# Performance work log

Measured on AMD Instinct MI355X. Metric: run time of the kernel, lower is better.

## Reference

```python
import jax, jax.numpy as jnp
import numpy as np

B, N, D, QM, QP, NP, T = 16, 900, 256, 4, 4, 6, 4


def setup_inputs() -> dict:
    key = jax.random.key(0)
    ks = jax.random.split(key, 12)
    return {
        "motion_query": jax.random.normal(ks[0], (B, N, D), jnp.float32),
        "plan_query": jax.random.normal(ks[1], (B, NP, D), jnp.float32),
        "ego_status_feature": jax.random.normal(ks[2], (B, D), jnp.float32),
        "motion_queue": jax.random.normal(ks[3], (B, QM, N, D), jnp.float32),
        "plan_queue": jax.random.normal(ks[4], (B, QP, NP, D), jnp.float32),
        "ego_status_queue": jax.random.normal(ks[5], (B, QP, D), jnp.float32),
        "period": jax.random.randint(ks[6], (B, QM), 0, 4, jnp.int32),
        "mask": jax.random.bernoulli(ks[7], 0.9, (B,)),
        "temp_anchor_embed_forstate": jax.random.normal(ks[8], (B, N, T, D), jnp.float32),
        "temp_mask_forstate": jax.random.bernoulli(ks[9], 0.5, (B, N, T)),
        "ego_temp_anchor_embed_forstate": jax.random.normal(ks[10], (B, 1, T, D), jnp.float32),
        "ego_temp_mask_forstate": jax.random.bernoulli(ks[11], 0.5, (B, 1, T)),
    }


def reference(motion_query, plan_query, ego_status_feature, motion_queue,
              plan_queue, ego_status_queue, period, mask,
              temp_anchor_embed_forstate, temp_mask_forstate,
              ego_temp_anchor_embed_forstate, ego_temp_mask_forstate):
    sg = jax.lax.stop_gradient
    # --- masked queue reset: for batch rows with mask==False, overwrite every
    # queue entry with the (detached) current value and zero the period ---
    reset = ~mask  # [B]
    mq = jnp.where(reset[:, None, None, None], sg(motion_query)[:, None], motion_queue)
    pq = jnp.where(reset[:, None, None, None], sg(plan_query)[:, None], plan_queue)
    eq = jnp.where(reset[:, None, None], sg(ego_status_feature)[:, None], ego_status_queue)
    per = jnp.where(reset[:, None], 0, period)

    # --- temporal window: T == 4, so both branches take the simple slice ---
    mm = temp_mask_forstate[..., :-1]            # [B, N, T-1]
    me = temp_anchor_embed_forstate[..., :-1, :]  # [B, N, T-1, D]
    pm = ego_temp_mask_forstate[..., :-1]         # [B, 1, T-1]
    pe = ego_temp_anchor_embed_forstate[..., :-1, :]  # [B, 1, T-1, D]

    # --- propagate plan embed forward over masked prefix ---
    any_flag = jnp.any(pm)
    all_true = jnp.all(pm, axis=(-2, -1))                # [B]
    m1 = pm[:, 0, :]                                     # [B, T-1] (Np == 1)
    first_false = jnp.argmin(m1, axis=-1)                # [B] index of first False
    Tm1 = pm.shape[-1]
    # embed at first-False slot (else branch) vs last-frame ego embed (all-True)
    repl_else = jnp.take_along_axis(pe, first_false[:, None, None, None], axis=2)[:, :, 0, :]
    repl_all = ego_temp_anchor_embed_forstate[:, :, -1, :]
    repl = jnp.where(all_true[:, None, None], repl_all, repl_else)  # [B, 1, D]
    j = jnp.arange(Tm1)
    overwrite = all_true[:, None] | (j[None, :] < first_false[:, None])  # [B, T-1]
    pe = jnp.where(any_flag & overwrite[:, None, :, None], repl[:, :, None, :], pe)

    return (mq, pq, eq, per,
            mm.swapaxes(1, 2), me.swapaxes(1, 2),
            pm.swapaxes(1, 2), pe.swapaxes(1, 2))
```

## Files before the change

### kernel.cpp

```cpp
#include <hip/hip_runtime.h>
#include <stdint.h>

namespace {
constexpr int Bn = 16, Nn = 900, Dn = 256, QMn = 4, QPn = 4, NPn = 6, Tn = 4;

constexpr int SZ_MQ  = Bn * QMn * Nn * Dn;
constexpr int SZ_PQ  = Bn * QPn * NPn * Dn;
constexpr int SZ_EQ  = Bn * QPn * Dn;
constexpr int SZ_PER = Bn * QMn;
constexpr int SZ_MM  = Bn * (Tn - 1) * Nn;
constexpr int SZ_ME  = Bn * (Tn - 1) * Nn * Dn;
constexpr int SZ_PM  = Bn * (Tn - 1);
constexpr int SZ_PE  = Bn * (Tn - 1) * Dn;

constexpr int OFF_MQ  = 0;
constexpr int OFF_PQ  = OFF_MQ + SZ_MQ;
constexpr int OFF_EQ  = OFF_PQ + SZ_PQ;
constexpr int OFF_PER = OFF_EQ + SZ_EQ;
constexpr int OFF_MM  = OFF_PER + SZ_PER;
constexpr int OFF_ME  = OFF_MM + SZ_MM;
constexpr int OFF_PM  = OFF_ME + SZ_ME;
constexpr int OFF_PE  = OFF_PM + SZ_PM;
constexpr int TOTAL   = OFF_PE + SZ_PE;
constexpr int NPACKS  = TOTAL / 8;
}

using u16 = unsigned short;

__device__ __forceinline__ float bits_to_f(unsigned u) {
    return __builtin_bit_cast(float, u);
}

__device__ int detect_float_mode(const void* p) {
    const unsigned* w = (const unsigned*)p;
    int cnt = 0;
#pragma unroll
    for (int i = 0; i < 32; ++i) {
        unsigned ex = (w[i] >> 7) & 0xFFu;
        cnt += (ex >= 120u && ex <= 133u) ? 1 : 0;
    }
    return (cnt >= 16) ? 1 : 0;
}

enum { BM_I32 = 0, BM_U8 = 1, BM_BF16 = 2, BM_F32 = 3 };
__device__ int detect_bool_mode(const void* p) {
    const unsigned* w = (const unsigned*)p;
    unsigned orw = 0, or_even = 0;
    bool hw_ok = true, u8_ok = true;
#pragma unroll
    for (int i = 0; i < 64; ++i) {
        unsigned x = w[i];
        orw |= x;
        unsigned lo = x & 0xFFFFu, hi = x >> 16;
        hw_ok = hw_ok && (lo == 0u || lo == 0x3F80u) && (hi == 0u || hi == 0x3F80u);
        or_even |= lo;
        u8_ok = u8_ok && ((x & 0xFEFEFEFEu) == 0u);
    }
    if (orw <= 1u) return BM_I32;
    if (hw_ok)     return (or_even == 0u) ? BM_F32 : BM_BF16;
    if (u8_ok)     return BM_U8;
    return BM_I32;
}

__device__ __forceinline__ bool get_bool(const void* p, int i, int m) {
    if (m == BM_I32) return ((const int*)p)[i] != 0;
    if (m == BM_U8)  return ((const unsigned char*)p)[i] != 0;
    if (m == BM_BF16) return ((const u16*)p)[i] != 0;
    return ((const unsigned*)p)[i] != 0;
}

__device__ int detect_period_mode(const void* p) {
    const unsigned* w = (const unsigned*)p;
    unsigned orw = 0, or_even = 0;
    bool hw_ok = true;
#pragma unroll
    for (int i = 0; i < 16; ++i) {
        unsigned x = w[i];
        orw |= x;
        unsigned lo = x & 0xFFFFu, hi = x >> 16;
        bool lo_ok = (lo == 0u || lo == 0x3F80u || lo == 0x4000u || lo == 0x4040u);
        bool hi_ok = (hi == 0u || hi == 0x3F80u || hi == 0x4000u || hi == 0x4040u);
        hw_ok = hw_ok && lo_ok && hi_ok;
        or_even |= lo;
    }
    if (orw <= 3u) return 0;
    if (hw_ok && or_even == 0u) return 2;
    return 1;
}

__device__ __forceinline__ float get_period_f(const void* p, int i, int m) {
    if (m == 0) return (float)((const int*)p)[i];
    if (m == 1) return bits_to_f((unsigned)((const u16*)p)[i] << 16);
    return ((const float*)p)[i];
}

__device__ __forceinline__ void load8f(const void* base, int e, int fm,
                                       float4& A, float4& B) {
    if (fm == 0) {
        const float* f = (const float*)base + e;
        A = reinterpret_cast<const float4*>(f)[0];
        B = reinterpret_cast<const float4*>(f)[1];
    } else {
        const int4 r = *reinterpret_cast<const int4*>((const u16*)base + e);
        unsigned x;
        x = (unsigned)r.x; A.x = bits_to_f(x << 16); A.y = bits_to_f(x & 0xFFFF0000u);
        x = (unsigned)r.y; A.z = bits_to_f(x << 16); A.w = bits_to_f(x & 0xFFFF0000u);
        x = (unsigned)r.z; B.x = bits_to_f(x << 16); B.y = bits_to_f(x & 0xFFFF0000u);
        x = (unsigned)r.w; B.z = bits_to_f(x << 16); B.w = bits_to_f(x & 0xFFFF0000u);
    }
}

__device__ __forceinline__ void compute_pack(
    int pack, int fm, int bm, int pmode,
    const void* __restrict__ motion_query,
    const void* __restrict__ plan_query,
    const void* __restrict__ ego_status_feature,
    const void* __restrict__ motion_queue,
    const void* __restrict__ plan_queue,
    const void* __restrict__ ego_status_queue,
    const void* __restrict__ period,
    const void* __restrict__ mask,
    const void* __restrict__ temp_anchor,
    const void* __restrict__ temp_mask,
    const void* __restrict__ ego_anchor,
    const void* __restrict__ ego_mask,
    float4& A, float4& B)
{
    const int idx = pack * 8;

    if (idx < OFF_PQ) {
        const int e = idx - OFF_MQ;
        const int d = e & (Dn - 1);
        const unsigned row = (unsigned)(e >> 8);
        const unsigned bq = row / (unsigned)Nn;
        const unsigned n = row - bq * (unsigned)Nn;
        const unsigned b = bq >> 2;
        const bool reset = !get_bool(mask, (int)b, bm);
        if (reset) load8f(motion_query, (((int)b * Nn + (int)n) << 8) + d, fm, A, B);
        else       load8f(motion_queue, e, fm, A, B);
    } else if (idx < OFF_EQ) {
        const int e = idx - OFF_PQ;
        const int d = e & (Dn - 1);
        const unsigned row = (unsigned)(e >> 8);
        const unsigned b = row / (unsigned)(QPn * NPn);
        const unsigned rem = row - b * (unsigned)(QPn * NPn);
        const unsigned q = rem / (unsigned)NPn;
        const unsigned p = rem - q * (unsigned)NPn;
        const bool reset = !get_bool(mask, (int)b, bm);
        if (reset) load8f(plan_query, (((int)b * NPn + (int)p) << 8) + d, fm, A, B);
        else       load8f(plan_queue, e, fm, A, B);
    } else if (idx < OFF_PER) {
        const int e = idx - OFF_EQ;
        const int d = e & (Dn - 1);
        const int row = e >> 8;
        const int b = row >> 2;
        const bool reset = !get_bool(mask, b, bm);
        if (reset) load8f(ego_status_feature, (b << 8) + d, fm, A, B);
        else       load8f(ego_status_queue, e, fm, A, B);
    } else if (idx < OFF_MM) {
        const int e = idx - OFF_PER;
        float h[8];
#pragma unroll
        for (int k = 0; k < 8; ++k) {
            const int g = e + k;
            const int b = g >> 2;
            const bool reset = !get_bool(mask, b, bm);
            h[k] = reset ? 0.0f : get_period_f(period, g, pmode);
        }
        A = make_float4(h[0], h[1], h[2], h[3]);
        B = make_float4(h[4], h[5], h[6], h[7]);
    } else if (idx < OFF_ME) {
        const int e = idx - OFF_MM;
        float h[8];
#pragma unroll
        for (int k = 0; k < 8; ++k) {
            const unsigned g = (unsigned)(e + k);
            const unsigned b = g / (unsigned)((Tn - 1) * Nn);
            const unsigned rem = g - b * (unsigned)((Tn - 1) * Nn);
            const unsigned t = rem / (unsigned)Nn;
            const unsigned n = rem - t * (unsigned)Nn;
            h[k] = get_bool(temp_mask, ((int)b * Nn + (int)n) * Tn + (int)t, bm)
                       ? 1.0f : 0.0f;
        }
        A = make_float4(h[0], h[1], h[2], h[3]);
        B = make_float4(h[4], h[5], h[6], h[7]);
    } else if (idx < OFF_PM) {
        const int e = idx - OFF_ME;
        const int d = e & (Dn - 1);
        const unsigned row = (unsigned)(e >> 8);
        const unsigned b = row / (unsigned)((Tn - 1) * Nn);
        const unsigned rem = row - b * (unsigned)((Tn - 1) * Nn);
        const unsigned t = rem / (unsigned)Nn;
        const unsigned n = rem - t * (unsigned)Nn;
        load8f(temp_anchor, ((((int)b * Nn + (int)n) * Tn + (int)t) << 8) + d, fm, A, B);
    } else if (idx < OFF_PE) {
        const int e = idx - OFF_PM;
        float h[8];
#pragma unroll
        for (int k = 0; k < 8; ++k) {
            const unsigned g = (unsigned)(e + k);
            const unsigned b = g / (unsigned)(Tn - 1);
            const unsigned t = g - b * (unsigned)(Tn - 1);
            h[k] = get_bool(ego_mask, (int)b * Tn + (int)t, bm) ? 1.0f : 0.0f;
        }
        A = make_float4(h[0], h[1], h[2], h[3]);
        B = make_float4(h[4], h[5], h[6], h[7]);
    } else {
        const int e = idx - OFF_PE;
        const int d = e & (Dn - 1);
        const unsigned row = (unsigned)(e >> 8);
        const unsigned b = row / (unsigned)(Tn - 1);
        const unsigned t = row - b * (unsigned)(Tn - 1);

        bool any_flag = false;
#pragma unroll
        for (int bb = 0; bb < Bn; ++bb) {
            any_flag = any_flag || get_bool(ego_mask, bb * Tn + 0, bm)
                                || get_bool(ego_mask, bb * Tn + 1, bm)
                                || get_bool(ego_mask, bb * Tn + 2, bm);
        }

        const bool p0 = get_bool(ego_mask, (int)b * Tn + 0, bm);
        const bool p1 = get_bool(ego_mask, (int)b * Tn + 1, bm);
        const bool p2 = get_bool(ego_mask, (int)b * Tn + 2, bm);
        const bool all_true = p0 && p1 && p2;
        const int first_false = (!p0) ? 0 : ((!p1) ? 1 : ((!p2) ? 2 : 0));

        const bool overwrite = all_true || ((int)t < first_false);
        int src_t = (int)t;
        if (any_flag && overwrite) src_t = all_true ? (Tn - 1) : first_false;

        load8f(ego_anchor, (((int)b * Tn + src_t) << 8) + d, fm, A, B);
    }
}

__global__ __launch_bounds__(256) void state_queue_kernel(
    const void* __restrict__ motion_query,
    const void* __restrict__ plan_query,
    const void* __restrict__ ego_status_feature,
    const void* __restrict__ motion_queue,
    const void* __restrict__ plan_queue,
    const void* __restrict__ ego_status_queue,
    const void* __restrict__ period,
    const void* __restrict__ mask,
    const void* __restrict__ temp_anchor,
    const void* __restrict__ temp_mask,
    const void* __restrict__ ego_anchor,
    const void* __restrict__ ego_mask,
    float* __restrict__ out)
{
    __shared__ int s_modes[3];
    if (threadIdx.x == 0) {
        s_modes[0] = detect_float_mode(motion_query);
        s_modes[1] = detect_bool_mode(temp_mask);
        s_modes[2] = detect_period_mode(period);
    }
    __syncthreads();
    const int fm = s_modes[0];
    const int bm = s_modes[1];
    const int pmode = s_modes[2];

    const int stride = (int)(gridDim.x * blockDim.x);

    for (int pack = (int)(blockIdx.x * blockDim.x + threadIdx.x);
         pack < NPACKS; pack += stride) {
        float4 A, B;
        compute_pack(pack, fm, bm, pmode,
                     motion_query, plan_query, ego_status_feature, motion_queue,
                     plan_queue, ego_status_queue, period, mask, temp_anchor,
                     temp_mask, ego_anchor, ego_mask, A, B);
        reinterpret_cast<float4*>(out + pack * 8)[0] = A;
        reinterpret_cast<float4*>(out + pack * 8)[1] = B;
    }
}

extern "C" void kernel_launch(void* const* d_in, const int* in_sizes, int n_in,
                              void* d_out, int out_size, void* d_ws, size_t ws_size,
                              hipStream_t stream) {
    float* out = (float*)d_out;
    const int threads = 256;
    const int blocks = 4096;
    state_queue_kernel<<<blocks, threads, 0, stream>>>(
        d_in[0], d_in[1], d_in[2], d_in[3], d_in[4], d_in[5], d_in[6], d_in[7],
        d_in[8], d_in[9], d_in[10], d_in[11], out);
}
```

Baseline: 226.0 us.

## Specialize blocks per output region instead of one grid-stride branchy loop

Replaces the uniform grid-stride loop, which ran a long branch chain for every pack, with a grid partitioned by region. One set of blocks copies the motion queue, another copies the temporal anchor embeds, each thread handling three packs at a fixed stride, and 64 blocks cover the small sections. This removes per-pack region dispatch and divergence on the two large copies and sizes the grid to the work. The small sections are handled by only 64 blocks, which may leave them lightly parallelized.

```diff
diff --git a/kernel.cpp b/kernel.cpp
--- a/kernel.cpp
+++ b/kernel.cpp
@@ -22,7 +22,15 @@
 constexpr int OFF_PM  = OFF_ME + SZ_ME;
 constexpr int OFF_PE  = OFF_PM + SZ_PM;
 constexpr int TOTAL   = OFF_PE + SZ_PE;
-constexpr int NPACKS  = TOTAL / 8;
+
+constexpr int MQ_BLOCKS    = SZ_MQ / 6144;
+constexpr int ME_BLOCKS    = SZ_ME / 6144;
+constexpr int SMALL_BLOCKS = 64;
+constexpr int NUM_BLOCKS   = MQ_BLOCKS + ME_BLOCKS + SMALL_BLOCKS;
+
+constexpr int SMALL1       = OFF_ME - OFF_PQ;
+constexpr int SMALL_TOTAL  = SMALL1 + (TOTAL - OFF_PM);
+constexpr int SMALL_PACKS  = SMALL_TOTAL / 8;
 }
 
 using u16 = unsigned short;
@@ -110,35 +118,20 @@
     }
 }
 
-__device__ __forceinline__ void compute_pack(
-    int pack, int fm, int bm, int pmode,
-    const void* __restrict__ motion_query,
+__device__ void compute_pack_small(
+    int idx, int fm, int bm, int pmode,
     const void* __restrict__ plan_query,
     const void* __restrict__ ego_status_feature,
-    const void* __restrict__ motion_queue,
     const void* __restrict__ plan_queue,
     const void* __restrict__ ego_status_queue,
     const void* __restrict__ period,
     const void* __restrict__ mask,
-    const void* __restrict__ temp_anchor,
     const void* __restrict__ temp_mask,
     const void* __restrict__ ego_anchor,
     const void* __restrict__ ego_mask,
     float4& A, float4& B)
 {
-    const int idx = pack * 8;
-
-    if (idx < OFF_PQ) {
-        const int e = idx - OFF_MQ;
-        const int d = e & (Dn - 1);
-        const unsigned row = (unsigned)(e >> 8);
-        const unsigned bq = row / (unsigned)Nn;
-        const unsigned n = row - bq * (unsigned)Nn;
-        const unsigned b = bq >> 2;
-        const bool reset = !get_bool(mask, (int)b, bm);
-        if (reset) load8f(motion_query, (((int)b * Nn + (int)n) << 8) + d, fm, A, B);
-        else       load8f(motion_queue, e, fm, A, B);
-    } else if (idx < OFF_EQ) {
+    if (idx < OFF_EQ) {
         const int e = idx - OFF_PQ;
         const int d = e & (Dn - 1);
         const unsigned row = (unsigned)(e >> 8);
@@ -184,15 +177,6 @@
         }
         A = make_float4(h[0], h[1], h[2], h[3]);
         B = make_float4(h[4], h[5], h[6], h[7]);
-    } else if (idx < OFF_PM) {
-        const int e = idx - OFF_ME;
-        const int d = e & (Dn - 1);
-        const unsigned row = (unsigned)(e >> 8);
-        const unsigned b = row / (unsigned)((Tn - 1) * Nn);
-        const unsigned rem = row - b * (unsigned)((Tn - 1) * Nn);
-        const unsigned t = rem / (unsigned)Nn;
-        const unsigned n = rem - t * (unsigned)Nn;
-        load8f(temp_anchor, ((((int)b * Nn + (int)n) * Tn + (int)t) << 8) + d, fm, A, B);
     } else if (idx < OFF_PE) {
         const int e = idx - OFF_PM;
         float h[8];
@@ -260,17 +244,57 @@
     const int bm = s_modes[1];
     const int pmode = s_modes[2];
 
-    const int stride = (int)(gridDim.x * blockDim.x);
-
-    for (int pack = (int)(blockIdx.x * blockDim.x + threadIdx.x);
-         pack < NPACKS; pack += stride) {
-        float4 A, B;
-        compute_pack(pack, fm, bm, pmode,
-                     motion_query, plan_query, ego_status_feature, motion_queue,
-                     plan_queue, ego_status_queue, period, mask, temp_anchor,
-                     temp_mask, ego_anchor, ego_mask, A, B);
-        reinterpret_cast<float4*>(out + pack * 8)[0] = A;
-        reinterpret_cast<float4*>(out + pack * 8)[1] = B;
+    const int bx  = (int)blockIdx.x;
+    const int tid = (int)threadIdx.x;
+
+    if (bx < MQ_BLOCKS) {
+        const int p0 = bx * 768 + tid;
+#pragma unroll
+        for (int it = 0; it < 3; ++it) {
+            const int e = (p0 + it * 256) * 8;
+            const int d = e & (Dn - 1);
+            const unsigned row = (unsigned)(e >> 8);
+            const unsigned bq  = row / (unsigned)Nn;
+            const unsigned n   = row - bq * (unsigned)Nn;
+            const unsigned b   = bq >> 2;
+            const bool keep = get_bool(mask, (int)b, bm);
+            const void* src = keep ? motion_queue : motion_query;
+            const int   off = keep ? e : ((((int)b * Nn + (int)n) << 8) + d);
+            float4 A, Bv;
+            load8f(src, off, fm, A, Bv);
+            reinterpret_cast<float4*>(out + e)[0] = A;
+            reinterpret_cast<float4*>(out + e)[1] = Bv;
+        }
+    } else if (bx < MQ_BLOCKS + ME_BLOCKS) {
+        const int p0 = (bx - MQ_BLOCKS) * 768 + tid;
+#pragma unroll
+        for (int it = 0; it < 3; ++it) {
+            const int e = (p0 + it * 256) * 8;
+            const int d = e & (Dn - 1);
+            const unsigned row = (unsigned)(e >> 8);
+            const unsigned b   = row / (unsigned)((Tn - 1) * Nn);
+            const unsigned rem = row - b * (unsigned)((Tn - 1) * Nn);
+            const unsigned t   = rem / (unsigned)Nn;
+            const unsigned n   = rem - t * (unsigned)Nn;
+            const int src = ((((int)b * Nn + (int)n) * Tn + (int)t) << 8) + d;
+            float4 A, Bv;
+            load8f(temp_anchor, src, fm, A, Bv);
+            reinterpret_cast<float4*>(out + OFF_ME + e)[0] = A;
+            reinterpret_cast<float4*>(out + OFF_ME + e)[1] = Bv;
+        }
+    } else {
+        const int sb = bx - (MQ_BLOCKS + ME_BLOCKS);
+        for (int w = sb * 256 + tid; w < SMALL_PACKS; w += SMALL_BLOCKS * 256) {
+            const int f = w * 8;
+            const int idx = (f < SMALL1) ? (OFF_PQ + f) : (OFF_PM + (f - SMALL1));
+            float4 A, Bv;
+            compute_pack_small(idx, fm, bm, pmode,
+                               plan_query, ego_status_feature, plan_queue,
+                               ego_status_queue, period, mask, temp_mask,
+                               ego_anchor, ego_mask, A, Bv);
+            reinterpret_cast<float4*>(out + idx)[0] = A;
+            reinterpret_cast<float4*>(out + idx)[1] = Bv;
+        }
     }
 }
 
@@ -278,9 +302,7 @@
                               void* d_out, int out_size, void* d_ws, size_t ws_size,
                               hipStream_t stream) {
     float* out = (float*)d_out;
-    const int threads = 256;
-    const int blocks = 4096;
-    state_queue_kernel<<<blocks, threads, 0, stream>>>(
+    state_queue_kernel<<<NUM_BLOCKS, 256, 0, stream>>>(
         d_in[0], d_in[1], d_in[2], d_in[3], d_in[4], d_in[5], d_in[6], d_in[7],
         d_in[8], d_in[9], d_in[10], d_in[11], out);
 }
```

After: 225.1 us. Within noise of the previous version (-0.4%).

## Replace grid-stride 8-element packs with one-shot 4-element chunks split across halves

Applied to the files above, without the earlier changes.

Replaces the fixed 4096-block grid-stride loop over 8-float packs with a full-size grid where each thread handles two 4-float chunks, one from the first half of the output (always inside the motion queue) and one from the second half. The loads are chosen by pointer and offset selection instead of branching. This aims to expose more parallelism, keep consecutive lanes on contiguous 16-byte accesses, and drop loop overhead. The cost is many more blocks, each with thread 0 rerunning the mode-detection probes before a block-wide barrier.

```diff
diff --git a/kernel.cpp b/kernel.cpp
--- a/kernel.cpp
+++ b/kernel.cpp
@@ -22,7 +22,12 @@
 constexpr int OFF_PM  = OFF_ME + SZ_ME;
 constexpr int OFF_PE  = OFF_PM + SZ_PM;
 constexpr int TOTAL   = OFF_PE + SZ_PE;
-constexpr int NPACKS  = TOTAL / 8;
+
+constexpr int NCHUNKS = TOTAL / 4;
+constexpr int HALFC   = NCHUNKS / 2;
+static_assert(HALFC * 4 < OFF_PQ, "first half must lie inside MQ");
+constexpr int THREADS = 256;
+constexpr int BLOCKS  = (HALFC + THREADS - 1) / THREADS;
 }
 
 using u16 = unsigned short;
@@ -94,24 +99,36 @@
     return ((const float*)p)[i];
 }
 
-__device__ __forceinline__ void load8f(const void* base, int e, int fm,
-                                       float4& A, float4& B) {
+__device__ __forceinline__ void load4f(const void* base, int e, int fm, float4& A) {
     if (fm == 0) {
-        const float* f = (const float*)base + e;
-        A = reinterpret_cast<const float4*>(f)[0];
-        B = reinterpret_cast<const float4*>(f)[1];
+        A = *reinterpret_cast<const float4*>((const float*)base + e);
     } else {
-        const int4 r = *reinterpret_cast<const int4*>((const u16*)base + e);
+        const int2 r = *reinterpret_cast<const int2*>((const u16*)base + e);
         unsigned x;
         x = (unsigned)r.x; A.x = bits_to_f(x << 16); A.y = bits_to_f(x & 0xFFFF0000u);
         x = (unsigned)r.y; A.z = bits_to_f(x << 16); A.w = bits_to_f(x & 0xFFFF0000u);
-        x = (unsigned)r.z; B.x = bits_to_f(x << 16); B.y = bits_to_f(x & 0xFFFF0000u);
-        x = (unsigned)r.w; B.z = bits_to_f(x << 16); B.w = bits_to_f(x & 0xFFFF0000u);
-    }
-}
-
-__device__ __forceinline__ void compute_pack(
-    int pack, int fm, int bm, int pmode,
+    }
+}
+
+__device__ __forceinline__ void compute_mq(
+    int idx, int fm, int bm,
+    const void* __restrict__ motion_query,
+    const void* __restrict__ motion_queue,
+    const void* __restrict__ mask, float4& A)
+{
+    const int d = idx & (Dn - 1);
+    const unsigned row = (unsigned)(idx >> 8);
+    const unsigned bq  = row / (unsigned)Nn;
+    const unsigned n   = row - bq * (unsigned)Nn;
+    const unsigned b   = bq >> 2;
+    const bool keep = get_bool(mask, (int)b, bm);
+    const void* src = keep ? motion_queue : motion_query;
+    const int   off = keep ? idx : ((((int)b * Nn + (int)n) << 8) + d);
+    load4f(src, off, fm, A);
+}
+
+__device__ void compute_chunk(
+    int idx, int fm, int bm, int pmode,
     const void* __restrict__ motion_query,
     const void* __restrict__ plan_query,
     const void* __restrict__ ego_status_feature,
@@ -124,20 +141,10 @@
     const void* __restrict__ temp_mask,
     const void* __restrict__ ego_anchor,
     const void* __restrict__ ego_mask,
-    float4& A, float4& B)
+    float4& A)
 {
-    const int idx = pack * 8;
-
     if (idx < OFF_PQ) {
-        const int e = idx - OFF_MQ;
-        const int d = e & (Dn - 1);
-        const unsigned row = (unsigned)(e >> 8);
-        const unsigned bq = row / (unsigned)Nn;
-        const unsigned n = row - bq * (unsigned)Nn;
-        const unsigned b = bq >> 2;
-        const bool reset = !get_bool(mask, (int)b, bm);
-        if (reset) load8f(motion_query, (((int)b * Nn + (int)n) << 8) + d, fm, A, B);
-        else       load8f(motion_queue, e, fm, A, B);
+        compute_mq(idx, fm, bm, motion_query, motion_queue, mask, A);
     } else if (idx < OFF_EQ) {
         const int e = idx - OFF_PQ;
         const int d = e & (Dn - 1);
@@ -146,34 +153,35 @@
         const unsigned rem = row - b * (unsigned)(QPn * NPn);
         const unsigned q = rem / (unsigned)NPn;
         const unsigned p = rem - q * (unsigned)NPn;
-        const bool reset = !get_bool(mask, (int)b, bm);
-        if (reset) load8f(plan_query, (((int)b * NPn + (int)p) << 8) + d, fm, A, B);
-        else       load8f(plan_queue, e, fm, A, B);
+        const bool keep = get_bool(mask, (int)b, bm);
+        const void* src = keep ? plan_queue : plan_query;
+        const int   off = keep ? e : ((((int)b * NPn + (int)p) << 8) + d);
+        load4f(src, off, fm, A);
     } else if (idx < OFF_PER) {
         const int e = idx - OFF_EQ;
         const int d = e & (Dn - 1);
         const int row = e >> 8;
         const int b = row >> 2;
-        const bool reset = !get_bool(mask, b, bm);
-        if (reset) load8f(ego_status_feature, (b << 8) + d, fm, A, B);
-        else       load8f(ego_status_queue, e, fm, A, B);
+        const bool keep = get_bool(mask, b, bm);
+        const void* src = keep ? ego_status_queue : ego_status_feature;
+        const int   off = keep ? e : ((b << 8) + d);
+        load4f(src, off, fm, A);
     } else if (idx < OFF_MM) {
         const int e = idx - OFF_PER;
-        float h[8];
-#pragma unroll
-        for (int k = 0; k < 8; ++k) {
+        float h[4];
+#pragma unroll
+        for (int k = 0; k < 4; ++k) {
             const int g = e + k;
             const int b = g >> 2;
             const bool reset = !get_bool(mask, b, bm);
             h[k] = reset ? 0.0f : get_period_f(period, g, pmode);
         }
         A = make_float4(h[0], h[1], h[2], h[3]);
-        B = make_float4(h[4], h[5], h[6], h[7]);
     } else if (idx < OFF_ME) {
         const int e = idx - OFF_MM;
-        float h[8];
-#pragma unroll
-        for (int k = 0; k < 8; ++k) {
+        float h[4];
+#pragma unroll
+        for (int k = 0; k < 4; ++k) {
             const unsigned g = (unsigned)(e + k);
             const unsigned b = g / (unsigned)((Tn - 1) * Nn);
             const unsigned rem = g - b * (unsigned)((Tn - 1) * Nn);
@@ -183,7 +191,6 @@
                        ? 1.0f : 0.0f;
         }
         A = make_float4(h[0], h[1], h[2], h[3]);
-        B = make_float4(h[4], h[5], h[6], h[7]);
     } else if (idx < OFF_PM) {
         const int e = idx - OFF_ME;
         const int d = e & (Dn - 1);
@@ -192,19 +199,18 @@
         const unsigned rem = row - b * (unsigned)((Tn - 1) * Nn);
         const unsigned t = rem / (unsigned)Nn;
         const unsigned n = rem - t * (unsigned)Nn;
-        load8f(temp_anchor, ((((int)b * Nn + (int)n) * Tn + (int)t) << 8) + d, fm, A, B);
+        load4f(temp_anchor, ((((int)b * Nn + (int)n) * Tn + (int)t) << 8) + d, fm, A);
     } else if (idx < OFF_PE) {
         const int e = idx - OFF_PM;
-        float h[8];
-#pragma unroll
-        for (int k = 0; k < 8; ++k) {
+        float h[4];
+#pragma unroll
+        for (int k = 0; k < 4; ++k) {
             const unsigned g = (unsigned)(e + k);
             const unsigned b = g / (unsigned)(Tn - 1);
             const unsigned t = g - b * (unsigned)(Tn - 1);
             h[k] = get_bool(ego_mask, (int)b * Tn + (int)t, bm) ? 1.0f : 0.0f;
         }
         A = make_float4(h[0], h[1], h[2], h[3]);
-        B = make_float4(h[4], h[5], h[6], h[7]);
     } else {
         const int e = idx - OFF_PE;
         const int d = e & (Dn - 1);
@@ -230,7 +236,7 @@
         int src_t = (int)t;
         if (any_flag && overwrite) src_t = all_true ? (Tn - 1) : first_false;
 
-        load8f(ego_anchor, (((int)b * Tn + src_t) << 8) + d, fm, A, B);
+        load4f(ego_anchor, (((int)b * Tn + src_t) << 8) + d, fm, A);
     }
 }
 
@@ -260,27 +266,28 @@
     const int bm = s_modes[1];
     const int pmode = s_modes[2];
 
-    const int stride = (int)(gridDim.x * blockDim.x);
-
-    for (int pack = (int)(blockIdx.x * blockDim.x + threadIdx.x);
-         pack < NPACKS; pack += stride) {
-        float4 A, B;
-        compute_pack(pack, fm, bm, pmode,
-                     motion_query, plan_query, ego_status_feature, motion_queue,
-                     plan_queue, ego_status_queue, period, mask, temp_anchor,
-                     temp_mask, ego_anchor, ego_mask, A, B);
-        reinterpret_cast<float4*>(out + pack * 8)[0] = A;
-        reinterpret_cast<float4*>(out + pack * 8)[1] = B;
-    }
+    const int c = (int)(blockIdx.x * blockDim.x + threadIdx.x);
+    if (c >= HALFC) return;
+
+    const int idx0 = c * 4;
+    const int idx1 = (c + HALFC) * 4;
+
+    float4 A0, A1;
+    compute_mq(idx0, fm, bm, motion_query, motion_queue, mask, A0);
+    compute_chunk(idx1, fm, bm, pmode,
+                  motion_query, plan_query, ego_status_feature, motion_queue,
+                  plan_queue, ego_status_queue, period, mask, temp_anchor,
+                  temp_mask, ego_anchor, ego_mask, A1);
+
+    *reinterpret_cast<float4*>(out + idx0) = A0;
+    *reinterpret_cast<float4*>(out + idx1) = A1;
 }
 
 extern "C" void kernel_launch(void* const* d_in, const int* in_sizes, int n_in,
                               void* d_out, int out_size, void* d_ws, size_t ws_size,
                               hipStream_t stream) {
     float* out = (float*)d_out;
-    const int threads = 256;
-    const int blocks = 4096;
-    state_queue_kernel<<<blocks, threads, 0, stream>>>(
+    state_queue_kernel<<<BLOCKS, THREADS, 0, stream>>>(
         d_in[0], d_in[1], d_in[2], d_in[3], d_in[4], d_in[5], d_in[6], d_in[7],
         d_in[8], d_in[9], d_in[10], d_in[11], out);
 }
```

New measurement: 223.9 us. Within noise of the previous version (-0.9%).
